# Optimization experiments

Hardware: AMD Instinct MI355X
Metric: run time of the kernel (lower is better)

Reference implementation:

```python
import jax, jax.numpy as jnp
import numpy as np

S, B, H = 2048, 32, 1024

def setup_inputs() -> dict:
    key = jax.random.key(0)
    k1, k2, k3 = jax.random.split(key, 3)
    hidden = jax.random.normal(k1, (1, B, H), dtype=jnp.float32)
    encoder_outputs = jax.random.normal(k2, (S, B, H), dtype=jnp.float32)
    W = jax.random.normal(k3, (H, H), dtype=jnp.float32) * (1.0 / np.sqrt(H))
    b = jnp.zeros((H,), dtype=jnp.float32)
    return {"hidden": hidden, "encoder_outputs": encoder_outputs, "W": W, "b": b}

def reference(hidden, encoder_outputs, W, b):
    # method == 'general': energy = Linear(enc_out); score = hidden . energy
    # Batched over all (b, s) pairs instead of the original python loop.
    proj = jnp.einsum('sbh,oh->sbo', encoder_outputs, W) + b  # [S,B,H]
    energies = jnp.einsum('bh,sbh->bs', hidden[0], proj)       # [B,S]
    attn = jax.nn.softmax(energies, axis=1)                    # softmax over seq
    return attn[:, None, :]                                    # [B,1,S]
```

## Files before the change

### kernel.cpp

```cpp
#include <hip/hip_runtime.h>

#define H 1024
#define S 2048
#define B 32

typedef float f4 __attribute__((ext_vector_type(4)));

__global__ __launch_bounds__(1024) void proj_hidden_kernel(
    const float* __restrict__ hidden, const float* __restrict__ W,
    float* __restrict__ v)
{
    const int tx = threadIdx.x & 15;
    const int ty = threadIdx.x >> 4;
    const int q  = blockIdx.x * 16 + tx;
    const int b0 = blockIdx.y * 2;
    const float4* W4 = reinterpret_cast<const float4*>(W);
    const float* h0 = hidden + b0 * H;
    const float* h1 = h0 + H;

    float4 a0 = {0.f, 0.f, 0.f, 0.f}, a1 = {0.f, 0.f, 0.f, 0.f};
#pragma unroll
    for (int i = 0; i < 16; ++i) {
        const int o = ty * 16 + i;
        const float4 w = W4[(size_t)o * (H / 4) + q];
        const float s0 = h0[o], s1 = h1[o];
        a0.x += s0 * w.x; a0.y += s0 * w.y; a0.z += s0 * w.z; a0.w += s0 * w.w;
        a1.x += s1 * w.x; a1.y += s1 * w.y; a1.z += s1 * w.z; a1.w += s1 * w.w;
    }

    __shared__ float4 red[32][16][2];
#pragma unroll
    for (int step = 32; step >= 1; step >>= 1) {
        if (ty >= step && ty < 2 * step) {
            red[ty - step][tx][0] = a0;
            red[ty - step][tx][1] = a1;
        }
        __syncthreads();
        if (ty < step) {
            const float4 r0 = red[ty][tx][0], r1 = red[ty][tx][1];
            a0.x += r0.x; a0.y += r0.y; a0.z += r0.z; a0.w += r0.w;
            a1.x += r1.x; a1.y += r1.y; a1.z += r1.z; a1.w += r1.w;
        }
        __syncthreads();
    }
    if (ty == 0) {
        reinterpret_cast<float4*>(v + (size_t)b0 * H)[q] = a0;
        reinterpret_cast<float4*>(v + (size_t)(b0 + 1) * H)[q] = a1;
    }
}

__global__ __launch_bounds__(256) void energies_kernel(
    const float* __restrict__ enc, const float* __restrict__ v,
    float* __restrict__ e)
{
    const int lane = threadIdx.x & 63;
    const int wave = threadIdx.x >> 6;
    const int b = blockIdx.y;
    const int s_base = blockIdx.x * 64 + wave * 16;

    const float4* v4 = reinterpret_cast<const float4*>(v + b * H);
    float4 vr[4];
#pragma unroll
    for (int k = 0; k < 4; ++k) vr[k] = v4[k * 64 + lane];

    float acc[16];
#pragma unroll
    for (int r = 0; r < 16; ++r) {
        const f4* e4 = reinterpret_cast<const f4*>(
            enc + ((size_t)(s_base + r) * B + b) * H);
        float a = 0.f;
#pragma unroll
        for (int k = 0; k < 4; ++k) {
            const f4 x = __builtin_nontemporal_load(e4 + k * 64 + lane);
            a += x[0] * vr[k].x + x[1] * vr[k].y + x[2] * vr[k].z + x[3] * vr[k].w;
        }
        acc[r] = a;
    }

    float t[8];
#pragma unroll
    for (int j = 0; j < 8; ++j) {
        const float a = acc[2 * j], c = acc[2 * j + 1];
        const float send = (lane & 1) ? a : c;
        const float recv = __shfl_xor(send, 1, 64);
        t[j] = ((lane & 1) ? c : a) + recv;
    }
#pragma unroll
    for (int j = 0; j < 4; ++j) {
        const float a = t[2 * j], c = t[2 * j + 1];
        const float send = (lane & 2) ? a : c;
        const float recv = __shfl_xor(send, 2, 64);
        t[j] = ((lane & 2) ? c : a) + recv;
    }
#pragma unroll
    for (int j = 0; j < 2; ++j) {
        const float a = t[2 * j], c = t[2 * j + 1];
        const float send = (lane & 4) ? a : c;
        const float recv = __shfl_xor(send, 4, 64);
        t[j] = ((lane & 4) ? c : a) + recv;
    }
    {
        const float a = t[0], c = t[1];
        const float send = (lane & 8) ? a : c;
        const float recv = __shfl_xor(send, 8, 64);
        t[0] = ((lane & 8) ? c : a) + recv;
    }
    t[0] += __shfl_xor(t[0], 16, 64);
    t[0] += __shfl_xor(t[0], 32, 64);

    if (lane < 16)
        e[b * S + s_base + lane] = t[0];
}

__global__ __launch_bounds__(256) void softmax_kernel(
    const float* __restrict__ e, float* __restrict__ out)
{
    const int b = blockIdx.x;
    const int tid = threadIdx.x;
    const int lane = tid & 63, wv = tid >> 6;

    float vals[8];
#pragma unroll
    for (int i = 0; i < 8; ++i) vals[i] = e[b * S + tid + i * 256];

    float m = vals[0];
#pragma unroll
    for (int i = 1; i < 8; ++i) m = fmaxf(m, vals[i]);
#pragma unroll
    for (int off = 32; off > 0; off >>= 1)
        m = fmaxf(m, __shfl_xor(m, off, 64));

    __shared__ float redm[4];
    __shared__ float reds[4];
    if (lane == 0) redm[wv] = m;
    __syncthreads();
    m = fmaxf(fmaxf(redm[0], redm[1]), fmaxf(redm[2], redm[3]));

    float sum = 0.f;
#pragma unroll
    for (int i = 0; i < 8; ++i) { vals[i] = __expf(vals[i] - m); sum += vals[i]; }
#pragma unroll
    for (int off = 32; off > 0; off >>= 1)
        sum += __shfl_xor(sum, off, 64);
    if (lane == 0) reds[wv] = sum;
    __syncthreads();
    sum = reds[0] + reds[1] + reds[2] + reds[3];

    const float inv = 1.f / sum;
#pragma unroll
    for (int i = 0; i < 8; ++i) out[b * S + tid + i * 256] = vals[i] * inv;
}

extern "C" void kernel_launch(void* const* d_in, const int* in_sizes, int n_in,
                              void* d_out, int out_size, void* d_ws, size_t ws_size,
                              hipStream_t stream) {
    const float* hidden = (const float*)d_in[0];
    const float* enc    = (const float*)d_in[1];
    const float* W      = (const float*)d_in[2];
    float* out = (float*)d_out;

    float* v = (float*)d_ws;
    float* e = v + B * H;

    proj_hidden_kernel<<<dim3(H / 64, B / 2), 1024, 0, stream>>>(hidden, W, v);
    energies_kernel<<<dim3(S / 64, B), 256, 0, stream>>>(enc, v, e);
    softmax_kernel<<<B, 256, 0, stream>>>(e, out);
}
```

Before: 53.67 us.

## Assign one sequence row per block in energies kernel, reducing across batch

The energies kernel now launches one block per sequence position. Each thread reads one float4 of every batch row from the contiguous 128KB encoder slice and the matching entry of v, so the enc stream is read fully sequentially per block. It then does a 32-way butterfly shuffle reduction and a cross-wave shared-memory reduction. In exchange, v (128KB) is re-read by every block instead of being held in registers, the stores to e are strided, and the nontemporal load hint on enc is dropped.

```diff
diff --git a/kernel.cpp b/kernel.cpp
--- a/kernel.cpp
+++ b/kernel.cpp
@@ -3,8 +3,6 @@
 #define H 1024
 #define S 2048
 #define B 32
-
-typedef float f4 __attribute__((ext_vector_type(4)));
 
 __global__ __launch_bounds__(1024) void proj_hidden_kernel(
     const float* __restrict__ hidden, const float* __restrict__ W,
@@ -53,63 +51,66 @@
     const float* __restrict__ enc, const float* __restrict__ v,
     float* __restrict__ e)
 {
-    const int lane = threadIdx.x & 63;
-    const int wave = threadIdx.x >> 6;
-    const int b = blockIdx.y;
-    const int s_base = blockIdx.x * 64 + wave * 16;
+    const int tid  = threadIdx.x;
+    const int lane = tid & 63;
+    const int wv   = tid >> 6;
+    const int s    = blockIdx.x;
 
-    const float4* v4 = reinterpret_cast<const float4*>(v + b * H);
-    float4 vr[4];
+    const float4* row4 = reinterpret_cast<const float4*>(enc) +
+                         (size_t)s * (B * H / 4);
+    const float4* v4 = reinterpret_cast<const float4*>(v);
+
+    float acc[B];
 #pragma unroll
-    for (int k = 0; k < 4; ++k) vr[k] = v4[k * 64 + lane];
-
-    float acc[16];
-#pragma unroll
-    for (int r = 0; r < 16; ++r) {
-        const f4* e4 = reinterpret_cast<const f4*>(
-            enc + ((size_t)(s_base + r) * B + b) * H);
-        float a = 0.f;
-#pragma unroll
-        for (int k = 0; k < 4; ++k) {
-            const f4 x = __builtin_nontemporal_load(e4 + k * 64 + lane);
-            a += x[0] * vr[k].x + x[1] * vr[k].y + x[2] * vr[k].z + x[3] * vr[k].w;
-        }
-        acc[r] = a;
+    for (int b = 0; b < B; ++b) {
+        const float4 x = row4[b * 256 + tid];
+        const float4 w = v4[b * 256 + tid];
+        acc[b] = x.x * w.x + x.y * w.y + x.z * w.z + x.w * w.w;
     }
 
-    float t[8];
+    float t[16];
 #pragma unroll
-    for (int j = 0; j < 8; ++j) {
+    for (int j = 0; j < 16; ++j) {
         const float a = acc[2 * j], c = acc[2 * j + 1];
         const float send = (lane & 1) ? a : c;
         const float recv = __shfl_xor(send, 1, 64);
         t[j] = ((lane & 1) ? c : a) + recv;
     }
 #pragma unroll
-    for (int j = 0; j < 4; ++j) {
+    for (int j = 0; j < 8; ++j) {
         const float a = t[2 * j], c = t[2 * j + 1];
         const float send = (lane & 2) ? a : c;
         const float recv = __shfl_xor(send, 2, 64);
         t[j] = ((lane & 2) ? c : a) + recv;
     }
 #pragma unroll
-    for (int j = 0; j < 2; ++j) {
+    for (int j = 0; j < 4; ++j) {
         const float a = t[2 * j], c = t[2 * j + 1];
         const float send = (lane & 4) ? a : c;
         const float recv = __shfl_xor(send, 4, 64);
         t[j] = ((lane & 4) ? c : a) + recv;
     }
+#pragma unroll
+    for (int j = 0; j < 2; ++j) {
+        const float a = t[2 * j], c = t[2 * j + 1];
+        const float send = (lane & 8) ? a : c;
+        const float recv = __shfl_xor(send, 8, 64);
+        t[j] = ((lane & 8) ? c : a) + recv;
+    }
     {
         const float a = t[0], c = t[1];
-        const float send = (lane & 8) ? a : c;
-        const float recv = __shfl_xor(send, 8, 64);
-        t[0] = ((lane & 8) ? c : a) + recv;
+        const float send = (lane & 16) ? a : c;
+        const float recv = __shfl_xor(send, 16, 64);
+        t[0] = ((lane & 16) ? c : a) + recv;
     }
-    t[0] += __shfl_xor(t[0], 16, 64);
     t[0] += __shfl_xor(t[0], 32, 64);
 
-    if (lane < 16)
-        e[b * S + s_base + lane] = t[0];
+    __shared__ float red[4][B];
+    if (lane < B) red[wv][lane] = t[0];
+    __syncthreads();
+    if (tid < B)
+        e[(size_t)tid * S + s] = red[0][tid] + red[1][tid] +
+                                 red[2][tid] + red[3][tid];
 }
 
 __global__ __launch_bounds__(256) void softmax_kernel(
@@ -163,6 +164,6 @@
     float* e = v + B * H;
 
     proj_hidden_kernel<<<dim3(H / 64, B / 2), 1024, 0, stream>>>(hidden, W, v);
-    energies_kernel<<<dim3(S / 64, B), 256, 0, stream>>>(enc, v, e);
+    energies_kernel<<<S, 256, 0, stream>>>(enc, v, e);
     softmax_kernel<<<B, 256, 0, stream>>>(e, out);
 }
```

New measurement: 53.65 us. Within noise of the previous version (-0.0%).

## Fuse softmax into energies kernel via last-block atomic counter

Applied to the files above, without the earlier changes.

Removes the separate softmax launch: each energies block bumps a per-batch atomic counter, and the last block to finish for a batch row runs the softmax over that row. The projection kernel now handles four batch rows per block instead of two and zeroes the counters. Nontemporal loads on the encoder stream are replaced with ordinary float4 loads. This saves a kernel launch and its gap, at the cost of fences, an atomic per block, and a serialized tail in which one block per batch does the softmax.

```diff
diff --git a/kernel.cpp b/kernel.cpp
--- a/kernel.cpp
+++ b/kernel.cpp
@@ -4,61 +4,74 @@
 #define S 2048
 #define B 32
 
-typedef float f4 __attribute__((ext_vector_type(4)));
-
 __global__ __launch_bounds__(1024) void proj_hidden_kernel(
     const float* __restrict__ hidden, const float* __restrict__ W,
-    float* __restrict__ v)
+    float* __restrict__ v, unsigned int* __restrict__ cnt)
 {
+    if (blockIdx.x == 0 && blockIdx.y == 0 && threadIdx.x < B)
+        cnt[threadIdx.x] = 0u;
+
     const int tx = threadIdx.x & 15;
     const int ty = threadIdx.x >> 4;
     const int q  = blockIdx.x * 16 + tx;
-    const int b0 = blockIdx.y * 2;
+    const int b0 = blockIdx.y * 4;
     const float4* W4 = reinterpret_cast<const float4*>(W);
-    const float* h0 = hidden + b0 * H;
+    const float* h0 = hidden + (size_t)b0 * H;
     const float* h1 = h0 + H;
+    const float* h2 = h1 + H;
+    const float* h3 = h2 + H;
 
-    float4 a0 = {0.f, 0.f, 0.f, 0.f}, a1 = {0.f, 0.f, 0.f, 0.f};
+    float4 a0 = {0,0,0,0}, a1 = {0,0,0,0}, a2 = {0,0,0,0}, a3 = {0,0,0,0};
 #pragma unroll
     for (int i = 0; i < 16; ++i) {
         const int o = ty * 16 + i;
         const float4 w = W4[(size_t)o * (H / 4) + q];
-        const float s0 = h0[o], s1 = h1[o];
+        const float s0 = h0[o], s1 = h1[o], s2 = h2[o], s3 = h3[o];
         a0.x += s0 * w.x; a0.y += s0 * w.y; a0.z += s0 * w.z; a0.w += s0 * w.w;
         a1.x += s1 * w.x; a1.y += s1 * w.y; a1.z += s1 * w.z; a1.w += s1 * w.w;
+        a2.x += s2 * w.x; a2.y += s2 * w.y; a2.z += s2 * w.z; a2.w += s2 * w.w;
+        a3.x += s3 * w.x; a3.y += s3 * w.y; a3.z += s3 * w.z; a3.w += s3 * w.w;
     }
 
-    __shared__ float4 red[32][16][2];
+    __shared__ float4 red[32][16][4];
 #pragma unroll
     for (int step = 32; step >= 1; step >>= 1) {
         if (ty >= step && ty < 2 * step) {
             red[ty - step][tx][0] = a0;
             red[ty - step][tx][1] = a1;
+            red[ty - step][tx][2] = a2;
+            red[ty - step][tx][3] = a3;
         }
         __syncthreads();
         if (ty < step) {
             const float4 r0 = red[ty][tx][0], r1 = red[ty][tx][1];
+            const float4 r2 = red[ty][tx][2], r3 = red[ty][tx][3];
             a0.x += r0.x; a0.y += r0.y; a0.z += r0.z; a0.w += r0.w;
             a1.x += r1.x; a1.y += r1.y; a1.z += r1.z; a1.w += r1.w;
+            a2.x += r2.x; a2.y += r2.y; a2.z += r2.z; a2.w += r2.w;
+            a3.x += r3.x; a3.y += r3.y; a3.z += r3.z; a3.w += r3.w;
         }
         __syncthreads();
     }
     if (ty == 0) {
-        reinterpret_cast<float4*>(v + (size_t)b0 * H)[q] = a0;
+        reinterpret_cast<float4*>(v + (size_t)(b0 + 0) * H)[q] = a0;
         reinterpret_cast<float4*>(v + (size_t)(b0 + 1) * H)[q] = a1;
+        reinterpret_cast<float4*>(v + (size_t)(b0 + 2) * H)[q] = a2;
+        reinterpret_cast<float4*>(v + (size_t)(b0 + 3) * H)[q] = a3;
     }
 }
 
 __global__ __launch_bounds__(256) void energies_kernel(
     const float* __restrict__ enc, const float* __restrict__ v,
-    float* __restrict__ e)
+    float* __restrict__ e, float* __restrict__ out,
+    unsigned int* __restrict__ cnt)
 {
     const int lane = threadIdx.x & 63;
     const int wave = threadIdx.x >> 6;
     const int b = blockIdx.y;
     const int s_base = blockIdx.x * 64 + wave * 16;
 
-    const float4* v4 = reinterpret_cast<const float4*>(v + b * H);
+    const float4* v4 = reinterpret_cast<const float4*>(v + (size_t)b * H);
     float4 vr[4];
 #pragma unroll
     for (int k = 0; k < 4; ++k) vr[k] = v4[k * 64 + lane];
@@ -66,13 +79,13 @@
     float acc[16];
 #pragma unroll
     for (int r = 0; r < 16; ++r) {
-        const f4* e4 = reinterpret_cast<const f4*>(
+        const float4* e4 = reinterpret_cast<const float4*>(
             enc + ((size_t)(s_base + r) * B + b) * H);
         float a = 0.f;
 #pragma unroll
         for (int k = 0; k < 4; ++k) {
-            const f4 x = __builtin_nontemporal_load(e4 + k * 64 + lane);
-            a += x[0] * vr[k].x + x[1] * vr[k].y + x[2] * vr[k].z + x[3] * vr[k].w;
+            const float4 x = e4[k * 64 + lane];
+            a += x.x * vr[k].x + x.y * vr[k].y + x.z * vr[k].z + x.w * vr[k].w;
         }
         acc[r] = a;
     }
@@ -109,19 +122,24 @@
     t[0] += __shfl_xor(t[0], 32, 64);
 
     if (lane < 16)
-        e[b * S + s_base + lane] = t[0];
-}
+        e[(size_t)b * S + s_base + lane] = t[0];
 
-__global__ __launch_bounds__(256) void softmax_kernel(
-    const float* __restrict__ e, float* __restrict__ out)
-{
-    const int b = blockIdx.x;
+    __shared__ int sdone;
+    __syncthreads();
+    if (threadIdx.x == 0) {
+        __threadfence();
+        const unsigned int old = atomicAdd(&cnt[b], 1u);
+        sdone = (old == (S / 64) - 1);
+    }
+    __syncthreads();
+    if (!sdone) return;
+    __threadfence();
+
     const int tid = threadIdx.x;
-    const int lane = tid & 63, wv = tid >> 6;
-
+    const int wv = wave;
     float vals[8];
 #pragma unroll
-    for (int i = 0; i < 8; ++i) vals[i] = e[b * S + tid + i * 256];
+    for (int i = 0; i < 8; ++i) vals[i] = e[(size_t)b * S + tid + i * 256];
 
     float m = vals[0];
 #pragma unroll
@@ -148,7 +166,8 @@
 
     const float inv = 1.f / sum;
 #pragma unroll
-    for (int i = 0; i < 8; ++i) out[b * S + tid + i * 256] = vals[i] * inv;
+    for (int i = 0; i < 8; ++i)
+        out[(size_t)b * S + tid + i * 256] = vals[i] * inv;
 }
 
 extern "C" void kernel_launch(void* const* d_in, const int* in_sizes, int n_in,
@@ -161,8 +180,8 @@
 
     float* v = (float*)d_ws;
     float* e = v + B * H;
+    unsigned int* cnt = (unsigned int*)(e + B * S);
 
-    proj_hidden_kernel<<<dim3(H / 64, B / 2), 1024, 0, stream>>>(hidden, W, v);
-    energies_kernel<<<dim3(S / 64, B), 256, 0, stream>>>(enc, v, e);
-    softmax_kernel<<<B, 256, 0, stream>>>(e, out);
+    proj_hidden_kernel<<<dim3(16, 8), 1024, 0, stream>>>(hidden, W, v, cnt);
+    energies_kernel<<<dim3(S / 64, B), 256, 0, stream>>>(enc, v, e, out, cnt);
 }
```

New measurement: 118.1 us. 2.2x slower.
